# Kernel optimization log

Hardware: AMD Instinct MI355X
Metric: run time of the kernel (lower is better)

## Reference

```python
import jax, jax.numpy as jnp
import numpy as np

N_NODES = 100000
N_EDGES = 1600000
F_IN = 128
N_GRAPHS = 1000
NUM_CLASSES = 2


def setup_inputs() -> dict:
    key = jax.random.key(0)
    ks = jax.random.split(key, 12)
    x = jax.random.normal(ks[0], (N_NODES, F_IN), jnp.float32)
    edge_index = jax.random.randint(ks[1], (2, N_EDGES), 0, N_NODES, dtype=jnp.int32)
    edge_weight = jnp.ones((N_EDGES,), jnp.float32)
    node_graph_index = jnp.sort(
        jax.random.randint(ks[2], (N_NODES,), 0, N_GRAPHS, dtype=jnp.int32))
    s = 0.05
    params = {
        'W0': jax.random.normal(ks[3], (F_IN, 64), jnp.float32) * s,
        'b0': jnp.zeros((64,), jnp.float32),
        'W1': jax.random.normal(ks[4], (64, 32), jnp.float32) * s,
        'b1': jnp.zeros((32,), jnp.float32),
        'Wm1': jax.random.normal(ks[5], (32, 128), jnp.float32) * s,
        'bm1': jnp.zeros((128,), jnp.float32),
        'Wm2': jax.random.normal(ks[6], (128, NUM_CLASSES), jnp.float32) * s,
        'bm2': jnp.zeros((NUM_CLASSES,), jnp.float32),
    }
    return dict(x=x, edge_index=edge_index, edge_weight=edge_weight,
                node_graph_index=node_graph_index, **params)


def _gcn_norm(edge_index, edge_weight, n_nodes):
    # renormalization trick: add self-loops, D^-1/2 (A+I) D^-1/2
    loop = jnp.arange(n_nodes, dtype=edge_index.dtype)
    src = jnp.concatenate([edge_index[0], loop])
    dst = jnp.concatenate([edge_index[1], loop])
    w = jnp.concatenate([edge_weight, jnp.ones((n_nodes,), edge_weight.dtype)])
    deg = jax.ops.segment_sum(w, dst, num_segments=n_nodes)
    dinv = jnp.where(deg > 0, jax.lax.rsqrt(jnp.maximum(deg, 1e-12)), 0.0)
    norm_w = dinv[src] * w * dinv[dst]
    return src, dst, norm_w


def _gcn_layer(h, src, dst, norm_w, W, b, n_nodes):
    m = h @ W                                # [N, out] dense transform first
    msg = m[src] * norm_w[:, None]           # [E+N, out] irregular gather
    agg = jax.ops.segment_sum(msg, dst, num_segments=n_nodes)
    return jax.nn.relu(agg + b)


def reference(x, edge_index, edge_weight, node_graph_index,
              W0, b0, W1, b1, Wm1, bm1, Wm2, bm2):
    n_nodes = x.shape[0]
    src, dst, norm_w = _gcn_norm(edge_index, edge_weight, n_nodes)
    h = _gcn_layer(x, src, dst, norm_w, W0, b0, n_nodes)   # GCN 64 + relu
    # dropout is identity at inference (training=False default)
    h = _gcn_layer(h, src, dst, norm_w, W1, b1, n_nodes)   # GCN 32 + relu
    g = jax.ops.segment_sum(h, node_graph_index, num_segments=N_GRAPHS)  # sum_pool
    g = jax.nn.relu(g @ Wm1 + bm1)
    logits = g @ Wm2 + bm2
    return logits
```

## Files before the change

### kernel.cpp

```cpp
#include <hip/hip_runtime.h>
#include <hip/hip_bf16.h>

#define F_IN 128
#define NPB 256
#define NPB_SH 8
#define MAXB 512
#define CHUNK 4096
#define CAPB 40
#define CAP 5120

typedef __attribute__((ext_vector_type(8))) short short8;
typedef __attribute__((ext_vector_type(4))) float f32x4;


__device__ __forceinline__ float bf2f(unsigned short u) {
    return __uint_as_float(((unsigned int)u) << 16);
}
__device__ __forceinline__ unsigned short f2bf(float f) {
    unsigned int x = __float_as_uint(f);
    x += 0x7FFFu + ((x >> 16) & 1u);
    return (unsigned short)(x >> 16);
}
__device__ __forceinline__ void bf8_fma(float w, uint4 r, float* a) {
    a[0] = fmaf(w, __uint_as_float(r.x << 16), a[0]);
    a[1] = fmaf(w, __uint_as_float(r.x & 0xFFFF0000u), a[1]);
    a[2] = fmaf(w, __uint_as_float(r.y << 16), a[2]);
    a[3] = fmaf(w, __uint_as_float(r.y & 0xFFFF0000u), a[3]);
    a[4] = fmaf(w, __uint_as_float(r.z << 16), a[4]);
    a[5] = fmaf(w, __uint_as_float(r.z & 0xFFFF0000u), a[5]);
    a[6] = fmaf(w, __uint_as_float(r.w << 16), a[6]);
    a[7] = fmaf(w, __uint_as_float(r.w & 0xFFFF0000u), a[7]);
}
__device__ __forceinline__ void fadd_global(float* p, float v) {
    unsafeAtomicAdd(p, v);
}

__global__ __launch_bounds__(1024) void bucket_prep_kernel(
    const int* __restrict__ src, const int* __restrict__ dst,
    const float* __restrict__ ew, int* __restrict__ cntkb,
    int2* __restrict__ tmp, const float* __restrict__ W0,
    unsigned short* __restrict__ W0t, float* __restrict__ Gbuf,
    int E, int nbucket, int nblk, int gtot) {
    __shared__ int hist[MAXB];
    const int tid = threadIdx.x;
    const int k = blockIdx.x;
    if (k == nblk) {
        for (int o = tid; o < 64 * 128; o += 1024) {
            int n = o >> 7, kk = o & 127;
            W0t[o] = f2bf(W0[kk * 64 + n]);
        }
        for (int o = tid; o < gtot; o += 1024) Gbuf[o] = 0.f;
        return;
    }
    const int e0 = k * CHUNK;
    const int e1 = min(e0 + CHUNK, E);
    for (int b = tid; b < nbucket; b += 1024) hist[b] = 0;
    __syncthreads();
    const size_t reg = (size_t)k * nbucket * CAPB;
    const int e = e0 + (tid << 2);
    if (e + 4 <= e1) {
        int4 d4 = *(const int4*)(dst + e);
        int4 s4 = *(const int4*)(src + e);
        float4 w4 = *(const float4*)(ew + e);
        {
            int d = d4.x, b = d >> NPB_SH;
            int r = atomicAdd(&hist[b], 1);
            if (r < CAPB) tmp[reg + (size_t)b * CAPB + r] =
                make_int2(s4.x | ((d & (NPB - 1)) << 17), __float_as_int(w4.x));
        }
        {
            int d = d4.y, b = d >> NPB_SH;
            int r = atomicAdd(&hist[b], 1);
            if (r < CAPB) tmp[reg + (size_t)b * CAPB + r] =
                make_int2(s4.y | ((d & (NPB - 1)) << 17), __float_as_int(w4.y));
        }
        {
            int d = d4.z, b = d >> NPB_SH;
            int r = atomicAdd(&hist[b], 1);
            if (r < CAPB) tmp[reg + (size_t)b * CAPB + r] =
                make_int2(s4.z | ((d & (NPB - 1)) << 17), __float_as_int(w4.z));
        }
        {
            int d = d4.w, b = d >> NPB_SH;
            int r = atomicAdd(&hist[b], 1);
            if (r < CAPB) tmp[reg + (size_t)b * CAPB + r] =
                make_int2(s4.w | ((d & (NPB - 1)) << 17), __float_as_int(w4.w));
        }
    } else {
        for (int j = e; j < e1; ++j) {
            int d = dst[j];
            int b = d >> NPB_SH;
            int r = atomicAdd(&hist[b], 1);
            if (r < CAPB) tmp[reg + (size_t)b * CAPB + r] =
                make_int2(src[j] | ((d & (NPB - 1)) << 17), __float_as_int(ew[j]));
        }
    }
    __syncthreads();
    for (int b = tid; b < nbucket; b += 1024)
        cntkb[(size_t)b * nblk + k] = min(hist[b], CAPB);
}

__global__ __launch_bounds__(1024) void csr_kernel(
    const int2* __restrict__ tmp, const int* __restrict__ cntkb,
    int2* __restrict__ es, int* __restrict__ rstart, int* __restrict__ rend,
    float* __restrict__ dinv, int N, int nbucket, int nblk) {
    __shared__ int ccs[MAXB];
    __shared__ int cnt[256];
    __shared__ float dw[256];
    __shared__ int off[256];
    __shared__ int cur[256];
    const int t = threadIdx.x;
    const int b = blockIdx.x;
    const int n0 = b << NPB_SH;
    const size_t seg = (size_t)b * CAP;
    if (t < 256) {
        cnt[t] = 0;
        dw[t] = 0.f;
    }
    for (int k = t; k < nblk; k += 1024) ccs[k] = cntkb[(size_t)b * nblk + k];
    __syncthreads();
    const int tot = nblk * CAPB;
    for (int s = t; s < tot; s += 1024) {
        int k = s / CAPB, j = s - k * CAPB;
        if (j < ccs[k]) {
            int2 e2 = tmp[((size_t)k * nbucket + b) * CAPB + j];
            int d = e2.x >> 17;
            atomicAdd(&cnt[d], 1);
            atomicAdd(&dw[d], __int_as_float(e2.y));
        }
    }
    __syncthreads();
    if (t < 256) off[t] = cnt[t];
    __syncthreads();
    for (int o = 1; o < 256; o <<= 1) {
        int x = 0;
        if (t >= o && t < 256) x = off[t - o];
        __syncthreads();
        if (t < 256) off[t] += x;
        __syncthreads();
    }
    if (t < 256) {
        int v = cnt[t];
        int excl = off[t] - v;
        cur[t] = excl;
        int n = n0 + t;
        if (n < N) {
            rstart[n] = (int)seg + excl;
            rend[n] = (int)seg + excl + v;
            dinv[n] = rsqrtf(fmaxf(1.f + dw[t], 1e-12f));
        }
    }
    __syncthreads();
    for (int s = t; s < tot; s += 1024) {
        int k = s / CAPB, j = s - k * CAPB;
        if (j < ccs[k]) {
            int2 e2 = tmp[((size_t)k * nbucket + b) * CAPB + j];
            int d = e2.x >> 17;
            int r = atomicAdd(&cur[d], 1);
            es[seg + r] = make_int2(e2.x & 0x1FFFF, e2.y);
        }
    }
}

__global__ __launch_bounds__(256) void gemm1_mfma_kernel(
    const float* __restrict__ X, const unsigned short* __restrict__ W0t,
    const float* __restrict__ dinv, unsigned short* __restrict__ M, int N) {
    __shared__ unsigned short Bs[64][136];
    const int tid = threadIdx.x;
    for (int i = tid; i < 64 * 32; i += 256) {
        int n = i >> 5, k4 = i & 31;
        ushort4 v = ((const ushort4*)W0t)[i];
        *(ushort4*)&Bs[n][k4 * 4] = v;
    }
    __syncthreads();
    const int wave = tid >> 6, lane = tid & 63;
    const int m = lane & 15, q = lane >> 4;
    const int rowA = blockIdx.x * 64 + wave * 16 + m;
    const bool rok = rowA < N;
    const float* xrow = X + (size_t)rowA * 128;
    f32x4 acc[4] = {};
#pragma unroll
    for (int ks = 0; ks < 4; ++ks) {
        int k0 = ks * 32 + q * 8;
        float4 u0 = make_float4(0.f, 0.f, 0.f, 0.f);
        float4 u1 = make_float4(0.f, 0.f, 0.f, 0.f);
        if (rok) {
            u0 = *(const float4*)(xrow + k0);
            u1 = *(const float4*)(xrow + k0 + 4);
        }
        short8 a;
        a[0] = (short)f2bf(u0.x); a[1] = (short)f2bf(u0.y);
        a[2] = (short)f2bf(u0.z); a[3] = (short)f2bf(u0.w);
        a[4] = (short)f2bf(u1.x); a[5] = (short)f2bf(u1.y);
        a[6] = (short)f2bf(u1.z); a[7] = (short)f2bf(u1.w);
#pragma unroll
        for (int ct = 0; ct < 4; ++ct) {
            short8 b = *(const short8*)&Bs[ct * 16 + m][k0];
            acc[ct] = __builtin_amdgcn_mfma_f32_16x16x32_bf16(a, b, acc[ct], 0, 0, 0);
        }
    }
#pragma unroll
    for (int r = 0; r < 4; ++r) {
        int crow = blockIdx.x * 64 + wave * 16 + q * 4 + r;
        if (crow < N) {
            float d = dinv[crow];
#pragma unroll
            for (int ct = 0; ct < 4; ++ct)
                M[(size_t)crow * 64 + ct * 16 + m] = f2bf(acc[ct][r] * d);
        }
    }
}

__global__ __launch_bounds__(256) void pull1_l2_kernel(
    const int* __restrict__ rstart, const int* __restrict__ rend,
    const int2* __restrict__ es, const unsigned short* __restrict__ M,
    const float* __restrict__ dinv, const float* __restrict__ bias,
    const float* __restrict__ W1, unsigned short* __restrict__ m1p, int N) {
    __shared__ float w1s[64 * 32];
    __shared__ float h1s[8 * 64];
    __shared__ float sdv[8];
    const int t = threadIdx.x;
    for (int i = t; i < 64 * 32; i += 256) w1s[i] = W1[i];
    const int lane = t & 63;
    const int d = t >> 5;
    const int node = blockIdx.x * 8 + d;
    const int c = lane & 7;
    const int q = (lane >> 3) & 3;
    const bool valid = node < N;
    if (valid) {
        float acc[8] = {0.f, 0.f, 0.f, 0.f, 0.f, 0.f, 0.f, 0.f};
        if (q == 0) {
            uint4 r = *(const uint4*)(M + (size_t)node * 64 + c * 8);
            bf8_fma(1.f, r, acc);
        }
        const int b = rstart[node], e = rend[node];
        const int len = e - b;
        const int base = len >> 2, rem = len & 3;
        int p = b + q * base + min(q, rem);
        const int pe = p + base + (q < rem ? 1 : 0);
        for (; p + 2 <= pe; p += 2) {
            int4 v = *(const int4*)(es + p);
            uint4 r0 = *(const uint4*)(M + (size_t)v.x * 64 + c * 8);
            uint4 r1 = *(const uint4*)(M + (size_t)v.z * 64 + c * 8);
            bf8_fma(__int_as_float(v.y), r0, acc);
            bf8_fma(__int_as_float(v.w), r1, acc);
        }
        if (p < pe) {
            int2 ed = es[p];
            uint4 r = *(const uint4*)(M + (size_t)ed.x * 64 + c * 8);
            bf8_fma(__int_as_float(ed.y), r, acc);
        }
#pragma unroll
        for (int off = 8; off <= 16; off <<= 1)
#pragma unroll
            for (int k = 0; k < 8; ++k) acc[k] += __shfl_xor(acc[k], off);
        if (q == 0) {
            float dv = dinv[node];
            const float* bp = bias + c * 8;
            float4 b0v = *(const float4*)(bp);
            float4 b1v = *(const float4*)(bp + 4);
            float* hp = h1s + d * 64 + c * 8;
            hp[0] = fmaxf(fmaf(dv, acc[0], b0v.x), 0.f);
            hp[1] = fmaxf(fmaf(dv, acc[1], b0v.y), 0.f);
            hp[2] = fmaxf(fmaf(dv, acc[2], b0v.z), 0.f);
            hp[3] = fmaxf(fmaf(dv, acc[3], b0v.w), 0.f);
            hp[4] = fmaxf(fmaf(dv, acc[4], b1v.x), 0.f);
            hp[5] = fmaxf(fmaf(dv, acc[5], b1v.y), 0.f);
            hp[6] = fmaxf(fmaf(dv, acc[6], b1v.z), 0.f);
            hp[7] = fmaxf(fmaf(dv, acc[7], b1v.w), 0.f);
            if (c == 0) sdv[d] = dv;
        }
    }
    __syncthreads();
    if (valid) {
        const int n = t & 31;
        const float* hp = h1s + d * 64;
        float a2 = 0.f;
#pragma unroll
        for (int k = 0; k < 64; ++k) a2 = fmaf(hp[k], w1s[k * 32 + n], a2);
        m1p[(size_t)node * 32 + n] = f2bf(sdv[d] * a2);
    }
}

__global__ __launch_bounds__(256) void pull2_pool_kernel(
    const int* __restrict__ rstart, const int* __restrict__ rend,
    const int2* __restrict__ es, const unsigned short* __restrict__ M,
    const float* __restrict__ dinv, const float* __restrict__ bias,
    const int* __restrict__ ngi, float* __restrict__ g, int N) {
    __shared__ float4 sh[16][8];
    __shared__ int sgx[16];
    const int t = threadIdx.x;
    const int lane = t & 63;
    const int nl = t >> 4;
    const int node = blockIdx.x * 16 + nl;
    const int c = lane & 3;
    const int q = (lane >> 2) & 3;
    const bool valid = node < N;
    float acc[8] = {0.f, 0.f, 0.f, 0.f, 0.f, 0.f, 0.f, 0.f};
    if (valid) {
        if (q == 0) {
            uint4 r = *(const uint4*)(M + (size_t)node * 32 + c * 8);
            bf8_fma(1.f, r, acc);
        }
        const int b = rstart[node], e = rend[node];
        const int len = e - b;
        const int base = len >> 2, rem = len & 3;
        int p = b + q * base + min(q, rem);
        const int pe = p + base + (q < rem ? 1 : 0);
        for (; p + 2 <= pe; p += 2) {
            int4 v = *(const int4*)(es + p);
            uint4 r0 = *(const uint4*)(M + (size_t)v.x * 32 + c * 8);
            uint4 r1 = *(const uint4*)(M + (size_t)v.z * 32 + c * 8);
            bf8_fma(__int_as_float(v.y), r0, acc);
            bf8_fma(__int_as_float(v.w), r1, acc);
        }
        if (p < pe) {
            int2 ed = es[p];
            uint4 r = *(const uint4*)(M + (size_t)ed.x * 32 + c * 8);
            bf8_fma(__int_as_float(ed.y), r, acc);
        }
#pragma unroll
        for (int off = 4; off <= 8; off <<= 1)
#pragma unroll
            for (int k = 0; k < 8; ++k) acc[k] += __shfl_xor(acc[k], off);
    }
    if (q == 0) {
        float4 o0 = make_float4(0.f, 0.f, 0.f, 0.f);
        float4 o1 = make_float4(0.f, 0.f, 0.f, 0.f);
        if (valid) {
            float d = dinv[node];
            const float* bp = bias + c * 8;
            float4 b0v = *(const float4*)(bp);
            float4 b1v = *(const float4*)(bp + 4);
            o0.x = fmaxf(fmaf(d, acc[0], b0v.x), 0.f);
            o0.y = fmaxf(fmaf(d, acc[1], b0v.y), 0.f);
            o0.z = fmaxf(fmaf(d, acc[2], b0v.z), 0.f);
            o0.w = fmaxf(fmaf(d, acc[3], b0v.w), 0.f);
            o1.x = fmaxf(fmaf(d, acc[4], b1v.x), 0.f);
            o1.y = fmaxf(fmaf(d, acc[5], b1v.y), 0.f);
            o1.z = fmaxf(fmaf(d, acc[6], b1v.z), 0.f);
            o1.w = fmaxf(fmaf(d, acc[7], b1v.w), 0.f);
        }
        sh[nl][c * 2] = o0;
        sh[nl][c * 2 + 1] = o1;
        if (c == 0) sgx[nl] = valid ? ngi[node] : -1;
    }
    __syncthreads();
    if (t < 8) {
        int cc = t;
        float4 a = make_float4(0.f, 0.f, 0.f, 0.f);
        int cg = -1;
        for (int i = 0; i < 16; ++i) {
            int gi = sgx[i];
            if (gi < 0) continue;
            if (gi != cg) {
                if (cg >= 0) {
                    float* gp = g + cg * 32 + cc * 4;
                    fadd_global(gp + 0, a.x); fadd_global(gp + 1, a.y);
                    fadd_global(gp + 2, a.z); fadd_global(gp + 3, a.w);
                }
                cg = gi;
                a = sh[i][cc];
            } else {
                float4 tv = sh[i][cc];
                a.x += tv.x; a.y += tv.y; a.z += tv.z; a.w += tv.w;
            }
        }
        if (cg >= 0) {
            float* gp = g + cg * 32 + cc * 4;
            fadd_global(gp + 0, a.x); fadd_global(gp + 1, a.y);
            fadd_global(gp + 2, a.z); fadd_global(gp + 3, a.w);
        }
    }
}

__global__ __launch_bounds__(128) void mlp_kernel(
    const float* __restrict__ g, const float* __restrict__ Wm1,
    const float* __restrict__ bm1, const float* __restrict__ Wm2,
    const float* __restrict__ bm2, float* __restrict__ out) {
    __shared__ float sg[32];
    __shared__ float red[4];
    int b = blockIdx.x, t = threadIdx.x;
    if (t < 32) sg[t] = g[b * 32 + t];
    __syncthreads();
    float acc = bm1[t];
#pragma unroll
    for (int k = 0; k < 32; ++k) acc = fmaf(sg[k], Wm1[k * 128 + t], acc);
    float h = fmaxf(acc, 0.f);
    float p0 = h * Wm2[t * 2 + 0];
    float p1 = h * Wm2[t * 2 + 1];
#pragma unroll
    for (int off = 32; off >= 1; off >>= 1) {
        p0 += __shfl_xor(p0, off);
        p1 += __shfl_xor(p1, off);
    }
    if ((t & 63) == 0) {
        red[(t >> 6) * 2 + 0] = p0;
        red[(t >> 6) * 2 + 1] = p1;
    }
    __syncthreads();
    if (t < 2) out[b * 2 + t] = bm2[t] + red[t] + red[2 + t];
}


extern "C" void kernel_launch(void* const* d_in, const int* in_sizes, int n_in,
                              void* d_out, int out_size, void* d_ws, size_t ws_size,
                              hipStream_t stream) {
    const float* x   = (const float*)d_in[0];
    const int*   ei  = (const int*)d_in[1];
    const float* ew  = (const float*)d_in[2];
    const int*   ngi = (const int*)d_in[3];
    const float* W0  = (const float*)d_in[4];
    const float* b0  = (const float*)d_in[5];
    const float* W1  = (const float*)d_in[6];
    const float* b1  = (const float*)d_in[7];
    const float* Wm1 = (const float*)d_in[8];
    const float* bm1 = (const float*)d_in[9];
    const float* Wm2 = (const float*)d_in[10];
    const float* bm2 = (const float*)d_in[11];
    float* out = (float*)d_out;

    const int N = in_sizes[0] / F_IN;
    const int E = in_sizes[1] / 2;
    const int G = out_size / 2;
    const int* srcp = ei;
    const int* dstp = ei + E;
    const int NBUCKET = (N + NPB - 1) >> NPB_SH;
    const int NBLK = (E + CHUNK - 1) / CHUNK;

    char* wsb = (char*)d_ws;
    size_t off = 0;
    auto alloc = [&](size_t bytes) {
        char* p = wsb + off;
        off += (bytes + 255) & ~(size_t)255;
        return p;
    };
    float* dinv     = (float*)alloc((size_t)N * 4);
    int*   rstart   = (int*)  alloc((size_t)N * 4);
    int*   rend     = (int*)  alloc((size_t)N * 4);
    int*   cntkb    = (int*)  alloc((size_t)NBUCKET * NBLK * 4);
    int2*  tmp      = (int2*) alloc((size_t)NBLK * NBUCKET * CAPB * 8);
    int2*  es       = (int2*) alloc((size_t)NBUCKET * CAP * 8);
    unsigned short* W0t = (unsigned short*)alloc(64 * 128 * 2);
    unsigned short* M   = (unsigned short*)alloc((size_t)N * 64 * 2);
    unsigned short* m1p = (unsigned short*)alloc((size_t)N * 32 * 2);
    float* Gbuf     = (float*)alloc((size_t)G * 32 * 4);

    bucket_prep_kernel<<<NBLK + 1, 1024, 0, stream>>>(
        srcp, dstp, ew, cntkb, tmp, W0, W0t, Gbuf, E, NBUCKET, NBLK, G * 32);
    csr_kernel<<<NBUCKET, 1024, 0, stream>>>(tmp, cntkb, es, rstart, rend, dinv, N, NBUCKET, NBLK);

    gemm1_mfma_kernel<<<(N + 63) / 64, 256, 0, stream>>>(x, W0t, dinv, M, N);

    pull1_l2_kernel<<<(N + 7) / 8, 256, 0, stream>>>(rstart, rend, es, M, dinv, b0, W1, m1p, N);

    pull2_pool_kernel<<<(N + 15) / 16, 256, 0, stream>>>(rstart, rend, es, m1p, dinv, b1, ngi, Gbuf, N);
    mlp_kernel<<<G, 128, 0, stream>>>(Gbuf, Wm1, bm1, Wm2, bm2, out);
}
```

Measured before the change: 244.6 us.

## Fuse CSR build with first GEMM and unroll edge gathers by four

The first layer's dense transform is merged into the CSR construction kernel. Each 1024-thread block, which owns 256 destination nodes, now also computes those nodes' X·W0 rows with MFMA and scales them by dinv values held in shared memory. This removes one kernel launch and a global dinv read. The pull kernels' edge loops are unrolled to four edges per iteration so more row gathers are in flight at once, and the edge-list and temp reads now use nontemporal loads. In exchange, the fused kernel needs more shared memory and runs its GEMM on only NBUCKET blocks, which may lower parallelism for that phase.

Result: slower. 261.4 us (+6.8%).

```diff
diff --git a/kernel.cpp b/kernel.cpp
--- a/kernel.cpp
+++ b/kernel.cpp
@@ -11,6 +11,8 @@
 
 typedef __attribute__((ext_vector_type(8))) short short8;
 typedef __attribute__((ext_vector_type(4))) float f32x4;
+typedef __attribute__((ext_vector_type(4))) int int4v;
+typedef __attribute__((ext_vector_type(2))) int int2v;
 
 
 __device__ __forceinline__ float bf2f(unsigned short u) {
@@ -100,22 +102,31 @@
         cntkb[(size_t)b * nblk + k] = min(hist[b], CAPB);
 }
 
-__global__ __launch_bounds__(1024) void csr_kernel(
+__global__ __launch_bounds__(1024) void csr_gemm1_kernel(
     const int2* __restrict__ tmp, const int* __restrict__ cntkb,
+    const float* __restrict__ X, const unsigned short* __restrict__ W0t,
     int2* __restrict__ es, int* __restrict__ rstart, int* __restrict__ rend,
-    float* __restrict__ dinv, int N, int nbucket, int nblk) {
+    float* __restrict__ dinv, unsigned short* __restrict__ M,
+    int N, int nbucket, int nblk) {
     __shared__ int ccs[MAXB];
     __shared__ int cnt[256];
-    __shared__ float dw[256];
+    __shared__ float dwv[256];
     __shared__ int off[256];
     __shared__ int cur[256];
+    __shared__ float dvs[256];
+    __shared__ unsigned short Bs[64][136];
     const int t = threadIdx.x;
     const int b = blockIdx.x;
     const int n0 = b << NPB_SH;
     const size_t seg = (size_t)b * CAP;
+    for (int i = t; i < 64 * 32; i += 1024) {
+        int nn = i >> 5, k4 = i & 31;
+        ushort4 v = ((const ushort4*)W0t)[i];
+        *(ushort4*)&Bs[nn][k4 * 4] = v;
+    }
     if (t < 256) {
         cnt[t] = 0;
-        dw[t] = 0.f;
+        dwv[t] = 0.f;
     }
     for (int k = t; k < nblk; k += 1024) ccs[k] = cntkb[(size_t)b * nblk + k];
     __syncthreads();
@@ -123,10 +134,11 @@
     for (int s = t; s < tot; s += 1024) {
         int k = s / CAPB, j = s - k * CAPB;
         if (j < ccs[k]) {
-            int2 e2 = tmp[((size_t)k * nbucket + b) * CAPB + j];
+            int2v e2 = __builtin_nontemporal_load(
+                (const int2v*)(tmp + ((size_t)k * nbucket + b) * CAPB + j));
             int d = e2.x >> 17;
             atomicAdd(&cnt[d], 1);
-            atomicAdd(&dw[d], __int_as_float(e2.y));
+            atomicAdd(&dwv[d], __int_as_float(e2.y));
         }
     }
     __syncthreads();
@@ -144,38 +156,29 @@
         int excl = off[t] - v;
         cur[t] = excl;
         int n = n0 + t;
+        float dv = rsqrtf(fmaxf(1.f + dwv[t], 1e-12f));
+        dvs[t] = dv;
         if (n < N) {
             rstart[n] = (int)seg + excl;
             rend[n] = (int)seg + excl + v;
-            dinv[n] = rsqrtf(fmaxf(1.f + dw[t], 1e-12f));
+            dinv[n] = dv;
         }
     }
     __syncthreads();
     for (int s = t; s < tot; s += 1024) {
         int k = s / CAPB, j = s - k * CAPB;
         if (j < ccs[k]) {
-            int2 e2 = tmp[((size_t)k * nbucket + b) * CAPB + j];
+            int2v e2 = __builtin_nontemporal_load(
+                (const int2v*)(tmp + ((size_t)k * nbucket + b) * CAPB + j));
             int d = e2.x >> 17;
             int r = atomicAdd(&cur[d], 1);
             es[seg + r] = make_int2(e2.x & 0x1FFFF, e2.y);
         }
     }
-}
-
-__global__ __launch_bounds__(256) void gemm1_mfma_kernel(
-    const float* __restrict__ X, const unsigned short* __restrict__ W0t,
-    const float* __restrict__ dinv, unsigned short* __restrict__ M, int N) {
-    __shared__ unsigned short Bs[64][136];
-    const int tid = threadIdx.x;
-    for (int i = tid; i < 64 * 32; i += 256) {
-        int n = i >> 5, k4 = i & 31;
-        ushort4 v = ((const ushort4*)W0t)[i];
-        *(ushort4*)&Bs[n][k4 * 4] = v;
-    }
-    __syncthreads();
-    const int wave = tid >> 6, lane = tid & 63;
+    const int wave = t >> 6, lane = t & 63;
     const int m = lane & 15, q = lane >> 4;
-    const int rowA = blockIdx.x * 64 + wave * 16 + m;
+    const int rowL = wave * 16 + m;
+    const int rowA = n0 + rowL;
     const bool rok = rowA < N;
     const float* xrow = X + (size_t)rowA * 128;
     f32x4 acc[4] = {};
@@ -195,18 +198,19 @@
         a[6] = (short)f2bf(u1.z); a[7] = (short)f2bf(u1.w);
 #pragma unroll
         for (int ct = 0; ct < 4; ++ct) {
-            short8 b = *(const short8*)&Bs[ct * 16 + m][k0];
-            acc[ct] = __builtin_amdgcn_mfma_f32_16x16x32_bf16(a, b, acc[ct], 0, 0, 0);
+            short8 bb = *(const short8*)&Bs[ct * 16 + m][k0];
+            acc[ct] = __builtin_amdgcn_mfma_f32_16x16x32_bf16(a, bb, acc[ct], 0, 0, 0);
         }
     }
 #pragma unroll
     for (int r = 0; r < 4; ++r) {
-        int crow = blockIdx.x * 64 + wave * 16 + q * 4 + r;
+        int cl = wave * 16 + q * 4 + r;
+        int crow = n0 + cl;
         if (crow < N) {
-            float d = dinv[crow];
+            float dv = dvs[cl];
 #pragma unroll
             for (int ct = 0; ct < 4; ++ct)
-                M[(size_t)crow * 64 + ct * 16 + m] = f2bf(acc[ct][r] * d);
+                M[(size_t)crow * 64 + ct * 16 + m] = f2bf(acc[ct][r] * dv);
         }
     }
 }
@@ -238,12 +242,25 @@
         const int base = len >> 2, rem = len & 3;
         int p = b + q * base + min(q, rem);
         const int pe = p + base + (q < rem ? 1 : 0);
-        for (; p + 2 <= pe; p += 2) {
-            int4 v = *(const int4*)(es + p);
+        for (; p + 4 <= pe; p += 4) {
+            int4v v0 = __builtin_nontemporal_load((const int4v*)(es + p));
+            int4v v1 = __builtin_nontemporal_load((const int4v*)(es + p + 2));
+            uint4 r0 = *(const uint4*)(M + (size_t)v0.x * 64 + c * 8);
+            uint4 r1 = *(const uint4*)(M + (size_t)v0.z * 64 + c * 8);
+            uint4 r2 = *(const uint4*)(M + (size_t)v1.x * 64 + c * 8);
+            uint4 r3 = *(const uint4*)(M + (size_t)v1.z * 64 + c * 8);
+            bf8_fma(__int_as_float(v0.y), r0, acc);
+            bf8_fma(__int_as_float(v0.w), r1, acc);
+            bf8_fma(__int_as_float(v1.y), r2, acc);
+            bf8_fma(__int_as_float(v1.w), r3, acc);
+        }
+        if (p + 2 <= pe) {
+            int4v v = __builtin_nontemporal_load((const int4v*)(es + p));
             uint4 r0 = *(const uint4*)(M + (size_t)v.x * 64 + c * 8);
             uint4 r1 = *(const uint4*)(M + (size_t)v.z * 64 + c * 8);
             bf8_fma(__int_as_float(v.y), r0, acc);
             bf8_fma(__int_as_float(v.w), r1, acc);
+            p += 2;
         }
         if (p < pe) {
             int2 ed = es[p];
@@ -307,12 +324,25 @@
         const int base = len >> 2, rem = len & 3;
         int p = b + q * base + min(q, rem);
         const int pe = p + base + (q < rem ? 1 : 0);
-        for (; p + 2 <= pe; p += 2) {
-            int4 v = *(const int4*)(es + p);
+        for (; p + 4 <= pe; p += 4) {
+            int4v v0 = __builtin_nontemporal_load((const int4v*)(es + p));
+            int4v v1 = __builtin_nontemporal_load((const int4v*)(es + p + 2));
+            uint4 r0 = *(const uint4*)(M + (size_t)v0.x * 32 + c * 8);
+            uint4 r1 = *(const uint4*)(M + (size_t)v0.z * 32 + c * 8);
+            uint4 r2 = *(const uint4*)(M + (size_t)v1.x * 32 + c * 8);
+            uint4 r3 = *(const uint4*)(M + (size_t)v1.z * 32 + c * 8);
+            bf8_fma(__int_as_float(v0.y), r0, acc);
+            bf8_fma(__int_as_float(v0.w), r1, acc);
+            bf8_fma(__int_as_float(v1.y), r2, acc);
+            bf8_fma(__int_as_float(v1.w), r3, acc);
+        }
+        if (p + 2 <= pe) {
+            int4v v = __builtin_nontemporal_load((const int4v*)(es + p));
             uint4 r0 = *(const uint4*)(M + (size_t)v.x * 32 + c * 8);
             uint4 r1 = *(const uint4*)(M + (size_t)v.z * 32 + c * 8);
             bf8_fma(__int_as_float(v.y), r0, acc);
             bf8_fma(__int_as_float(v.w), r1, acc);
+            p += 2;
         }
         if (p < pe) {
             int2 ed = es[p];
@@ -448,9 +478,8 @@
 
     bucket_prep_kernel<<<NBLK + 1, 1024, 0, stream>>>(
         srcp, dstp, ew, cntkb, tmp, W0, W0t, Gbuf, E, NBUCKET, NBLK, G * 32);
-    csr_kernel<<<NBUCKET, 1024, 0, stream>>>(tmp, cntkb, es, rstart, rend, dinv, N, NBUCKET, NBLK);
-
-    gemm1_mfma_kernel<<<(N + 63) / 64, 256, 0, stream>>>(x, W0t, dinv, M, N);
+    csr_gemm1_kernel<<<NBUCKET, 1024, 0, stream>>>(
+        tmp, cntkb, x, W0t, es, rstart, rend, dinv, M, N, NBUCKET, NBLK);
 
     pull1_l2_kernel<<<(N + 7) / 8, 256, 0, stream>>>(rstart, rend, es, M, dinv, b0, W1, m1p, N);
 
```
